# Kernel optimization log

Measured on AMD Instinct MI355X. Metric: run time of the kernel, lower is better.

Reference implementation:

```python
import jax, jax.numpy as jnp
import numpy as np

BITS = 4
MAXQ = (1 << BITS) - 1          # 15
PACK = 32 // BITS               # 8 values per int32
GROUP = 128
CLIPMIN = 1e-5
CLIPMAX = 1e4


def _unpack_rows(qweight, infeatures):
    # qweight: [in/PACK, out] int32; values packed along the row (infeatures) dim.
    shifts = (jnp.arange(PACK, dtype=jnp.int32) * BITS)[None, :, None]   # [1,PACK,1]
    w = (qweight[:, None, :] >> shifts) & MAXQ                            # [in/PACK, PACK, out]
    return w.reshape(-1, qweight.shape[1])[:infeatures].astype(jnp.float32)


def setup_inputs() -> dict:
    key = jax.random.key(0)
    k1, k2, k3, k4, k5 = jax.random.split(key, 5)
    infeatures, outfeatures, tokens = 4096, 4096, 2048
    num_groups = infeatures // GROUP
    x = jax.random.normal(k1, (tokens, infeatures), dtype=jnp.float32)
    # positive scales, well inside [CLIPMIN, CLIPMAX]
    scales = jax.random.uniform(k2, (num_groups, outfeatures), dtype=jnp.float32,
                                minval=0.005, maxval=0.02)
    # zero points roughly centered in the quant range [0, 15]
    zero_points = jax.random.uniform(k3, (num_groups, outfeatures), dtype=jnp.float32,
                                     minval=0.0, maxval=float(MAXQ))
    bias = jax.random.normal(k4, (outfeatures,), dtype=jnp.float32)
    qweight = jax.random.randint(k5, (infeatures // PACK, outfeatures),
                                 jnp.iinfo(jnp.int32).min, jnp.iinfo(jnp.int32).max,
                                 dtype=jnp.int32)
    return {"x": x, "scales": scales, "zero_points": zero_points,
            "bias": bias, "qweight": qweight}


def reference(x, scales, zero_points, bias, qweight):
    infeatures = x.shape[-1]
    out_f = scales.shape[1]
    num_groups = scales.shape[0]
    w = _unpack_rows(qweight, infeatures)                       # [in, out] fp32 in [0,15]
    s = jnp.clip(scales, CLIPMIN, CLIPMAX)                      # [G, out]
    z = jnp.clip(jnp.round(zero_points), 0.0, float(MAXQ))      # [G, out]
    wg = w.reshape(num_groups, GROUP, out_f)                    # [G, group, out]
    deq = ((wg - z[:, None, :]) * s[:, None, :]).reshape(infeatures, out_f)
    return x @ deq + bias
```

## Files before the change

### kernel.cpp

```cpp
#include <hip/hip_runtime.h>
#include <cstdint>
#include <cstddef>

typedef __attribute__((ext_vector_type(2))) _Float16 half2v;
typedef __attribute__((ext_vector_type(8))) _Float16 half8;
typedef __attribute__((ext_vector_type(4))) float floatx4;

typedef __attribute__((address_space(1))) const void gvoid_t;
typedef __attribute__((address_space(3))) void lvoid_t;

__global__ __launch_bounds__(256) void convert_x_kernel(
    const float* __restrict__ x, _Float16* __restrict__ xh, long long n)
{
    long long i = ((long long)blockIdx.x * 256 + threadIdx.x) * 8;
    if (i + 8 > n) return;
    const float4* p = (const float4*)(x + i);
    float4 a = p[0];
    float4 b = p[1];
    half8 h;
    h[0] = (_Float16)a.x; h[1] = (_Float16)b.x;
    h[2] = (_Float16)a.y; h[3] = (_Float16)b.y;
    h[4] = (_Float16)a.z; h[5] = (_Float16)b.z;
    h[6] = (_Float16)a.w; h[7] = (_Float16)b.w;
    *(half8*)(xh + i) = h;
}

#define BM 128
#define BN 128
#define BK 64

__device__ inline half8 unpack8(int q, half2v sh, half2v ch)
{
    unsigned uq = (unsigned)q;
    unsigned p0 = (uq & 0x000F000Fu) | 0x64006400u;
    unsigned p1 = ((uq >> 4) & 0x000F000Fu) | 0x64006400u;
    unsigned p2 = ((uq >> 8) & 0x000F000Fu) | 0x64006400u;
    unsigned p3 = ((uq >> 12) & 0x000F000Fu) | 0x64006400u;
    half2v v0 = (__builtin_bit_cast(half2v, p0) - ch) * sh;
    half2v v1 = (__builtin_bit_cast(half2v, p1) - ch) * sh;
    half2v v2 = (__builtin_bit_cast(half2v, p2) - ch) * sh;
    half2v v3 = (__builtin_bit_cast(half2v, p3) - ch) * sh;
    half8 r;
    r[0] = v0[0]; r[1] = v0[1]; r[2] = v1[0]; r[3] = v1[1];
    r[4] = v2[0]; r[5] = v2[1]; r[6] = v3[0]; r[7] = v3[1];
    return r;
}

__global__ __launch_bounds__(256) void gemm_fused(
    const _Float16* __restrict__ A, const int* __restrict__ qw,
    const float* __restrict__ scales, const float* __restrict__ zps,
    const float* __restrict__ bias, float* __restrict__ C,
    int M, int N, int K)
{
    __shared__ __align__(16) _Float16 a_lds[2][BM * BK];

    const int t  = threadIdx.x;
    const int L  = t & 63;
    const int w  = t >> 6;
    const int m0 = blockIdx.y * BM;
    const int n0 = blockIdx.x * BN;
    const int wm = (w & 1) * 64;
    const int wn = (w >> 1) * 64;

    floatx4 acc[4][4] = {};

    const int sr = L >> 3;
    const int sc = L & 7;
    const int gc = sc ^ sr;
    const _Float16* ag = A + (size_t)(m0 + w * 8 + sr) * K + gc * 8;
    const int dst = (w * 8) * BK;

    const int nc = n0 + wn + (L & 15);
    const int* qp = qw + (size_t)(L >> 4) * N + nc;
    const float* sp = scales + nc;
    const float* zp = zps + nc;

    const int NG = K / 128;

    #pragma unroll
    for (int i = 0; i < 4; ++i)
        __builtin_amdgcn_global_load_lds(
            (gvoid_t*)(ag + (size_t)i * 32 * K),
            (lvoid_t*)(&a_lds[0][dst + i * 32 * BK]), 16, 0, 0);

    int qc[8], qm[8];
    #pragma unroll
    for (int s2 = 0; s2 < 2; ++s2)
        #pragma unroll
        for (int j = 0; j < 4; ++j)
            qc[s2 * 4 + j] = qp[(size_t)(s2 * 4) * N + 16 * j];

    half2v sh[4], ch[4];
    {
        #pragma unroll
        for (int j = 0; j < 4; ++j) {
            float s = fminf(fmaxf(sp[16 * j], 1e-5f), 1e4f);
            float z = fminf(fmaxf(rintf(zp[16 * j]), 0.0f), 15.0f);
            _Float16 hs = (_Float16)s;
            _Float16 hc = (_Float16)(1024.0f + z);
            sh[j][0] = hs; sh[j][1] = hs;
            ch[j][0] = hc; ch[j][1] = hc;
        }
    }

    auto compute = [&](int cur, const int* qarr) {
        #pragma unroll
        for (int s2 = 0; s2 < 2; ++s2) {
            const int p = (s2 * 4 + (L >> 4)) ^ (L & 7);
            half8 af[4];
            #pragma unroll
            for (int i = 0; i < 4; ++i)
                af[i] = *(const half8*)(&a_lds[cur][(wm + 16 * i + (L & 15)) * BK + p * 8]);
            #pragma unroll
            for (int j = 0; j < 4; ++j) {
                half8 bf = unpack8(qarr[s2 * 4 + j], sh[j], ch[j]);
                #pragma unroll
                for (int i = 0; i < 4; ++i)
                    acc[i][j] = __builtin_amdgcn_mfma_f32_16x16x32_f16(
                        af[i], bf, acc[i][j], 0, 0, 0);
            }
        }
    };

    for (int g = 0; g < NG; ++g) {
        const int t1 = 2 * g + 1;

        __syncthreads();

        #pragma unroll
        for (int i = 0; i < 4; ++i)
            __builtin_amdgcn_global_load_lds(
                (gvoid_t*)(ag + (size_t)i * 32 * K + (size_t)t1 * BK),
                (lvoid_t*)(&a_lds[1][dst + i * 32 * BK]), 16, 0, 0);
        #pragma unroll
        for (int s2 = 0; s2 < 2; ++s2)
            #pragma unroll
            for (int j = 0; j < 4; ++j)
                qm[s2 * 4 + j] = qp[(size_t)(t1 * 8 + s2 * 4) * N + 16 * j];

        compute(0, qc);

        __syncthreads();

        float snf[4], znf[4];
        if (g + 1 < NG) {
            const int t2 = 2 * g + 2;
            #pragma unroll
            for (int i = 0; i < 4; ++i)
                __builtin_amdgcn_global_load_lds(
                    (gvoid_t*)(ag + (size_t)i * 32 * K + (size_t)t2 * BK),
                    (lvoid_t*)(&a_lds[0][dst + i * 32 * BK]), 16, 0, 0);
            #pragma unroll
            for (int s2 = 0; s2 < 2; ++s2)
                #pragma unroll
                for (int j = 0; j < 4; ++j)
                    qc[s2 * 4 + j] = qp[(size_t)(t2 * 8 + s2 * 4) * N + 16 * j];
            #pragma unroll
            for (int j = 0; j < 4; ++j) {
                snf[j] = sp[(size_t)(g + 1) * N + 16 * j];
                znf[j] = zp[(size_t)(g + 1) * N + 16 * j];
            }
        }

        compute(1, qm);

        if (g + 1 < NG) {
            #pragma unroll
            for (int j = 0; j < 4; ++j) {
                float s = fminf(fmaxf(snf[j], 1e-5f), 1e4f);
                float z = fminf(fmaxf(rintf(znf[j]), 0.0f), 15.0f);
                _Float16 hs = (_Float16)s;
                _Float16 hc = (_Float16)(1024.0f + z);
                sh[j][0] = hs; sh[j][1] = hs;
                ch[j][0] = hc; ch[j][1] = hc;
            }
        }
    }

    float bv[4];
    #pragma unroll
    for (int j = 0; j < 4; ++j)
        bv[j] = bias[nc + 16 * j];
    const int col0 = nc;
    #pragma unroll
    for (int i = 0; i < 4; ++i) {
        const int row0 = m0 + wm + 16 * i + (L >> 4) * 4;
        #pragma unroll
        for (int r = 0; r < 4; ++r) {
            float* outr = C + (size_t)(row0 + r) * N + col0;
            #pragma unroll
            for (int j = 0; j < 4; ++j)
                outr[16 * j] = acc[i][j][r] + bv[j];
        }
    }
}

extern "C" void kernel_launch(void* const* d_in, const int* in_sizes, int n_in,
                              void* d_out, int out_size, void* d_ws, size_t ws_size,
                              hipStream_t stream)
{
    const float* x      = (const float*)d_in[0];
    const float* scales = (const float*)d_in[1];
    const float* zps    = (const float*)d_in[2];
    const float* bias   = (const float*)d_in[3];
    const int*   qw     = (const int*)d_in[4];

    const int N = in_sizes[3];
    const int G = in_sizes[1] / N;
    const int K = G * 128;
    const int M = in_sizes[0] / K;

    _Float16* xh = (_Float16*)d_ws;
    float* out   = (float*)d_out;

    const long long nx = (long long)M * K;
    convert_x_kernel<<<(int)(nx / 2048), 256, 0, stream>>>(x, xh, nx);
    gemm_fused<<<dim3(N / BN, M / BM), 256, 0, stream>>>(
        xh, qw, scales, zps, bias, out, M, N, K);
}
```

Baseline: 193.4 us.

## Pre-dequantize weights into MFMA fragment layout in a separate kernel

Adds a kernel that dequantizes the int4 weights once into fp16, stored in the exact per-lane MFMA B-fragment order. The GEMM then loads ready fragments with contiguous 16-byte loads, with no unpack or scale/zero work inside the main loop. This removes the dequant that every M-tile repeated, at the cost of an extra launch, a larger fp16 weight read (4x the packed size) and more workspace. The grid order is also swapped so consecutive blocks walk along M and share the same weight columns.

```diff
diff --git a/kernel.cpp b/kernel.cpp
--- a/kernel.cpp
+++ b/kernel.cpp
@@ -24,10 +24,6 @@
     h[6] = (_Float16)a.w; h[7] = (_Float16)b.w;
     *(half8*)(xh + i) = h;
 }
-
-#define BM 128
-#define BN 128
-#define BK 64
 
 __device__ inline half8 unpack8(int q, half2v sh, half2v ch)
 {
@@ -46,9 +42,42 @@
     return r;
 }
 
-__global__ __launch_bounds__(256) void gemm_fused(
-    const _Float16* __restrict__ A, const int* __restrict__ qw,
-    const float* __restrict__ scales, const float* __restrict__ zps,
+__global__ __launch_bounds__(256) void dequant_frag_kernel(
+    const int* __restrict__ qw, const float* __restrict__ scales,
+    const float* __restrict__ zps, _Float16* __restrict__ Bf,
+    int N, int K)
+{
+    const int t = threadIdx.x, L = t & 63, w = t >> 6;
+    const int n16 = blockIdx.x;
+    const int n = n16 * 16 + (L & 15);
+    const int KF = K / 32;
+    const int f0 = blockIdx.y * 16;
+
+    #pragma unroll
+    for (int i = 0; i < 4; ++i) {
+        const int f = f0 + i * 4 + w;
+        const int r = f * 4 + (L >> 4);
+        const int q = qw[(size_t)r * N + n];
+        const int g = f >> 2;
+
+        float s = fminf(fmaxf(scales[(size_t)g * N + n], 1e-5f), 1e4f);
+        float z = fminf(fmaxf(rintf(zps[(size_t)g * N + n]), 0.0f), 15.0f);
+        _Float16 hs = (_Float16)s;
+        _Float16 hc = (_Float16)(1024.0f + z);
+        half2v sh; sh[0] = hs; sh[1] = hs;
+        half2v ch; ch[0] = hc; ch[1] = hc;
+
+        half8 h = unpack8(q, sh, ch);
+        *(half8*)(Bf + ((size_t)n16 * KF + f) * 512 + (size_t)L * 8) = h;
+    }
+}
+
+#define BM 128
+#define BN 128
+#define BK 64
+
+__global__ __launch_bounds__(256) void gemm_bfrag(
+    const _Float16* __restrict__ A, const _Float16* __restrict__ Bf,
     const float* __restrict__ bias, float* __restrict__ C,
     int M, int N, int K)
 {
@@ -57,8 +86,8 @@
     const int t  = threadIdx.x;
     const int L  = t & 63;
     const int w  = t >> 6;
-    const int m0 = blockIdx.y * BM;
-    const int n0 = blockIdx.x * BN;
+    const int m0 = blockIdx.x * BM;
+    const int n0 = blockIdx.y * BN;
     const int wm = (w & 1) * 64;
     const int wn = (w >> 1) * 64;
 
@@ -70,40 +99,28 @@
     const _Float16* ag = A + (size_t)(m0 + w * 8 + sr) * K + gc * 8;
     const int dst = (w * 8) * BK;
 
-    const int nc = n0 + wn + (L & 15);
-    const int* qp = qw + (size_t)(L >> 4) * N + nc;
-    const float* sp = scales + nc;
-    const float* zp = zps + nc;
-
-    const int NG = K / 128;
+    const int KF = K / 32;
+    const _Float16* bp[4];
+    #pragma unroll
+    for (int j = 0; j < 4; ++j)
+        bp[j] = Bf + ((size_t)(n0 / 16 + (w >> 1) * 4 + j) * KF) * 512
+                   + (size_t)L * 8;
+
+    const int NK = K / BK;
+    half8 b0[8], b1[8];
 
     #pragma unroll
     for (int i = 0; i < 4; ++i)
         __builtin_amdgcn_global_load_lds(
             (gvoid_t*)(ag + (size_t)i * 32 * K),
             (lvoid_t*)(&a_lds[0][dst + i * 32 * BK]), 16, 0, 0);
-
-    int qc[8], qm[8];
-    #pragma unroll
-    for (int s2 = 0; s2 < 2; ++s2)
-        #pragma unroll
-        for (int j = 0; j < 4; ++j)
-            qc[s2 * 4 + j] = qp[(size_t)(s2 * 4) * N + 16 * j];
-
-    half2v sh[4], ch[4];
-    {
-        #pragma unroll
-        for (int j = 0; j < 4; ++j) {
-            float s = fminf(fmaxf(sp[16 * j], 1e-5f), 1e4f);
-            float z = fminf(fmaxf(rintf(zp[16 * j]), 0.0f), 15.0f);
-            _Float16 hs = (_Float16)s;
-            _Float16 hc = (_Float16)(1024.0f + z);
-            sh[j][0] = hs; sh[j][1] = hs;
-            ch[j][0] = hc; ch[j][1] = hc;
-        }
-    }
-
-    auto compute = [&](int cur, const int* qarr) {
+    #pragma unroll
+    for (int j = 0; j < 4; ++j) {
+        b0[j * 2 + 0] = *(const half8*)(bp[j] + 0);
+        b0[j * 2 + 1] = *(const half8*)(bp[j] + 512);
+    }
+
+    auto compute = [&](int cur, const half8* barr) {
         #pragma unroll
         for (int s2 = 0; s2 < 2; ++s2) {
             const int p = (s2 * 4 + (L >> 4)) ^ (L & 7);
@@ -113,81 +130,59 @@
                 af[i] = *(const half8*)(&a_lds[cur][(wm + 16 * i + (L & 15)) * BK + p * 8]);
             #pragma unroll
             for (int j = 0; j < 4; ++j) {
-                half8 bf = unpack8(qarr[s2 * 4 + j], sh[j], ch[j]);
                 #pragma unroll
                 for (int i = 0; i < 4; ++i)
                     acc[i][j] = __builtin_amdgcn_mfma_f32_16x16x32_f16(
-                        af[i], bf, acc[i][j], 0, 0, 0);
+                        af[i], barr[j * 2 + s2], acc[i][j], 0, 0, 0);
             }
         }
     };
 
-    for (int g = 0; g < NG; ++g) {
-        const int t1 = 2 * g + 1;
-
+    for (int ti = 0; ti < NK; ti += 2) {
         __syncthreads();
-
-        #pragma unroll
-        for (int i = 0; i < 4; ++i)
-            __builtin_amdgcn_global_load_lds(
-                (gvoid_t*)(ag + (size_t)i * 32 * K + (size_t)t1 * BK),
-                (lvoid_t*)(&a_lds[1][dst + i * 32 * BK]), 16, 0, 0);
-        #pragma unroll
-        for (int s2 = 0; s2 < 2; ++s2)
-            #pragma unroll
-            for (int j = 0; j < 4; ++j)
-                qm[s2 * 4 + j] = qp[(size_t)(t1 * 8 + s2 * 4) * N + 16 * j];
-
-        compute(0, qc);
-
-        __syncthreads();
-
-        float snf[4], znf[4];
-        if (g + 1 < NG) {
-            const int t2 = 2 * g + 2;
+        {
+            const size_t kn = (size_t)(ti + 1) * BK;
             #pragma unroll
             for (int i = 0; i < 4; ++i)
                 __builtin_amdgcn_global_load_lds(
-                    (gvoid_t*)(ag + (size_t)i * 32 * K + (size_t)t2 * BK),
+                    (gvoid_t*)(ag + (size_t)i * 32 * K + kn),
+                    (lvoid_t*)(&a_lds[1][dst + i * 32 * BK]), 16, 0, 0);
+            #pragma unroll
+            for (int j = 0; j < 4; ++j) {
+                b1[j * 2 + 0] = *(const half8*)(bp[j] + (size_t)(ti + 1) * 1024);
+                b1[j * 2 + 1] = *(const half8*)(bp[j] + (size_t)(ti + 1) * 1024 + 512);
+            }
+        }
+        compute(0, b0);
+
+        __syncthreads();
+        if (ti + 2 < NK) {
+            const size_t kn = (size_t)(ti + 2) * BK;
+            #pragma unroll
+            for (int i = 0; i < 4; ++i)
+                __builtin_amdgcn_global_load_lds(
+                    (gvoid_t*)(ag + (size_t)i * 32 * K + kn),
                     (lvoid_t*)(&a_lds[0][dst + i * 32 * BK]), 16, 0, 0);
             #pragma unroll
-            for (int s2 = 0; s2 < 2; ++s2)
-                #pragma unroll
-                for (int j = 0; j < 4; ++j)
-                    qc[s2 * 4 + j] = qp[(size_t)(t2 * 8 + s2 * 4) * N + 16 * j];
-            #pragma unroll
             for (int j = 0; j < 4; ++j) {
-                snf[j] = sp[(size_t)(g + 1) * N + 16 * j];
-                znf[j] = zp[(size_t)(g + 1) * N + 16 * j];
+                b0[j * 2 + 0] = *(const half8*)(bp[j] + (size_t)(ti + 2) * 1024);
+                b0[j * 2 + 1] = *(const half8*)(bp[j] + (size_t)(ti + 2) * 1024 + 512);
             }
         }
-
-        compute(1, qm);
-
-        if (g + 1 < NG) {
-            #pragma unroll
-            for (int j = 0; j < 4; ++j) {
-                float s = fminf(fmaxf(snf[j], 1e-5f), 1e4f);
-                float z = fminf(fmaxf(rintf(znf[j]), 0.0f), 15.0f);
-                _Float16 hs = (_Float16)s;
-                _Float16 hc = (_Float16)(1024.0f + z);
-                sh[j][0] = hs; sh[j][1] = hs;
-                ch[j][0] = hc; ch[j][1] = hc;
-            }
-        }
-    }
-
+        compute(1, b1);
+    }
+
+    const int nc = n0 + wn + (L & 15);
     float bv[4];
     #pragma unroll
     for (int j = 0; j < 4; ++j)
         bv[j] = bias[nc + 16 * j];
-    const int col0 = nc;
     #pragma unroll
     for (int i = 0; i < 4; ++i) {
         const int row0 = m0 + wm + 16 * i + (L >> 4) * 4;
         #pragma unroll
         for (int r = 0; r < 4; ++r) {
-            float* outr = C + (size_t)(row0 + r) * N + col0;
+            float* outr = C + (size_t)(row0 + r) * N + nc;
             #pragma unroll
             for (int j = 0; j < 4; ++j)
                 outr[16 * j] = acc[i][j][r] + bv[j];
@@ -211,10 +206,13 @@
     const int M = in_sizes[0] / K;
 
     _Float16* xh = (_Float16*)d_ws;
+    _Float16* Bf = xh + (size_t)M * K;
     float* out   = (float*)d_out;
 
     const long long nx = (long long)M * K;
     convert_x_kernel<<<(int)(nx / 2048), 256, 0, stream>>>(x, xh, nx);
-    gemm_fused<<<dim3(N / BN, M / BM), 256, 0, stream>>>(
-        xh, qw, scales, zps, bias, out, M, N, K);
-}
+    dequant_frag_kernel<<<dim3(N / 16, K / 512), 256, 0, stream>>>(
+        qw, scales, zps, Bf, N, K);
+    gemm_bfrag<<<dim3(M / BM, N / BN), 256, 0, stream>>>(
+        xh, Bf, bias, out, M, N, K);
+}
```

Result: faster. 188.8 us (-2.4%).
